# Performance work log

Measured on AMD Instinct MI355X. Metric: run time of the kernel, lower is better.

The kernel has to match this reference:

```python
import jax, jax.numpy as jnp
import numpy as np

N_ROI = 1024
N_CLASS = 21      # num_classes + 1
APP_DIM = 1024
D_F = 128
N_REL = 16
DIM_K = 64
DIM_G = 64


def loc2bbox(src, loc):
    # src, loc: [M,4] with (y0,x0,y1,x1) / (dy,dx,dh,dw)
    h = src[:, 2] - src[:, 0]
    w = src[:, 3] - src[:, 1]
    cy = src[:, 0] + 0.5 * h
    cx = src[:, 1] + 0.5 * w
    ncy = loc[:, 0] * h + cy
    ncx = loc[:, 1] * w + cx
    nh = jnp.exp(loc[:, 2]) * h
    nw = jnp.exp(loc[:, 3]) * w
    return jnp.stack([ncy - 0.5 * nh, ncx - 0.5 * nw,
                      ncy + 0.5 * nh, ncx + 0.5 * nw], axis=1)


def rank_embedding(n, feat_dim, wave_len=1000.0):
    rank = jnp.arange(n, dtype=jnp.float32)[:, None]
    fr = jnp.arange(feat_dim // 2, dtype=jnp.float32)
    dim_mat = 1.0 / (wave_len ** (fr / (feat_dim / 2.0)))
    mul = rank * dim_mat[None, :]
    return jnp.concatenate([jnp.sin(mul), jnp.cos(mul)], axis=-1)  # [n, feat_dim]


def positional_embedding(f_g, dim_g, wave_len=1000.0):
    # f_g: [N,4]; replicates the repo's PositionalEmbedding exactly
    x_min, y_min, x_max, y_max = jnp.split(f_g, 4, axis=1)  # [N,1] each
    cx = (x_min + x_max) * 0.5
    cy = (y_min + y_max) * 0.5
    w = (x_max - x_min) + 1.0
    h = (y_max - y_min) + 1.0
    dx = jnp.log(jnp.maximum(jnp.abs((cx - cx.T) / w), 1e-3))
    dy = jnp.log(jnp.maximum(jnp.abs((cy - cy.T) / h), 1e-3))
    dw = jnp.log(w / w.T)
    dh = jnp.log(h / h.T)
    pos = jnp.stack([dx, dy, dw, dh], axis=-1)               # [N,N,4]
    fr = jnp.arange(dim_g // 8, dtype=jnp.float32)
    dim_mat = 1.0 / (wave_len ** (fr / (dim_g / 8.0)))       # [dim_g/8]
    mul = (100.0 * pos)[..., None] * dim_mat                 # [N,N,4,dim_g/8]
    mul = mul.reshape(pos.shape[0], pos.shape[1], -1)
    return jnp.concatenate([jnp.sin(mul), jnp.cos(mul)], axis=-1)  # [N,N,dim_g]


def setup_inputs():
    key = jax.random.key(0)
    ks = jax.random.split(key, 16)
    yx = jax.random.uniform(ks[0], (N_ROI, 2), minval=0.0, maxval=500.0)
    hw = jax.random.uniform(ks[1], (N_ROI, 2), minval=16.0, maxval=128.0)
    sample_roi = jnp.concatenate([yx, yx + hw], axis=1)      # valid (y0,x0,y1,x1)
    roi_cls_loc = jax.random.normal(ks[2], (N_ROI, N_CLASS * 4)) * 0.5
    roi_score = jax.random.normal(ks[3], (N_ROI, N_CLASS))
    # force no background argmax -> nonzero() filter keeps all N (static shapes)
    roi_score = roi_score.at[:, 0].add(-10.0)
    appearance_features = jax.random.normal(ks[4], (N_ROI, APP_DIM))
    size = jnp.array([600, 800], dtype=jnp.int32)
    s = 0.02
    rank_w = jax.random.normal(ks[5], (APP_DIM, D_F)) * s
    rank_b = jnp.zeros((D_F,), jnp.float32)
    feat_w = jax.random.normal(ks[6], (APP_DIM, D_F)) * s
    feat_b = jnp.zeros((D_F,), jnp.float32)
    logit_w = jax.random.normal(ks[7], (APP_DIM, 1)) * s
    logit_b = jnp.zeros((1,), jnp.float32)
    wg_w = jax.random.normal(ks[8], (N_REL, DIM_G)) * s
    wg_b = jnp.full((N_REL,), 0.1, jnp.float32)  # keep some geo weights > 0
    wk_w = jax.random.normal(ks[9], (N_REL, D_F, DIM_K)) * s
    wk_b = jnp.zeros((N_REL, DIM_K), jnp.float32)
    wq_w = jax.random.normal(ks[10], (N_REL, D_F, DIM_K)) * s
    wq_b = jnp.zeros((N_REL, DIM_K), jnp.float32)
    wv_w = jax.random.normal(ks[11], (N_REL, D_F, DIM_K)) * s
    wv_b = jnp.zeros((N_REL, DIM_K), jnp.float32)
    return {"sample_roi": sample_roi, "roi_cls_loc": roi_cls_loc,
            "roi_score": roi_score, "appearance_features": appearance_features,
            "size": size,
            "rank_w": rank_w, "rank_b": rank_b, "feat_w": feat_w, "feat_b": feat_b,
            "logit_w": logit_w, "logit_b": logit_b,
            "wg_w": wg_w, "wg_b": wg_b, "wk_w": wk_w, "wk_b": wk_b,
            "wq_w": wq_w, "wq_b": wq_b, "wv_w": wv_w, "wv_b": wv_b}


def reference(sample_roi, roi_cls_loc, roi_score, appearance_features, size,
              rank_w, rank_b, feat_w, feat_b, logit_w, logit_b,
              wg_w, wg_b, wk_w, wk_b, wq_w, wq_b, wv_w, wv_b):
    n = sample_roi.shape[0]
    size_f = size.astype(jnp.float32)
    # loc denormalization (mean = 0)
    std = jnp.tile(jnp.array([0.1, 0.1, 0.2, 0.2], jnp.float32), N_CLASS)
    loc = (roi_cls_loc * std).reshape(-1, 4)                  # [N*21,4]
    roi_rep = jnp.broadcast_to(sample_roi[:, None, :], (n, N_CLASS, 4)).reshape(-1, 4)
    cls_bbox = loc2bbox(roi_rep, loc).reshape(n, N_CLASS, 4)
    # replicates original's clamp on class-strided slices of the [N,21,4] view
    cls_bbox = cls_bbox.at[:, 0::2].set(jnp.clip(cls_bbox[:, 0::2], 0.0, size_f[0]))
    cls_bbox = cls_bbox.at[:, 1::2].set(jnp.clip(cls_bbox[:, 1::2], 0.0, size_f[1]))
    prob_all = jax.nn.softmax(roi_score, axis=1)
    prob = jnp.max(prob_all, axis=-1)
    prob_argmax = jnp.argmax(prob_all, axis=-1)
    cls_bbox = cls_bbox[jnp.arange(n), prob_argmax]           # [N,4]
    # background filter; inputs guarantee all foreground -> static size n
    nz = jnp.nonzero(prob_argmax, size=n, fill_value=0)[0]
    prob_argmax = prob_argmax[nz]
    prob = prob[nz]
    cls_bbox = cls_bbox[nz]
    feats = appearance_features[nz]
    order = jnp.argsort(-prob)                                # descending
    sorted_prob = prob[order]
    sorted_cls_bboxes = cls_bbox[order]
    sorted_labels = prob_argmax[order]
    sorted_features = feats[order]
    nms_rank = rank_embedding(n, APP_DIM) @ rank_w + rank_b   # [N,D_F]
    emb_feat = sorted_features @ feat_w + feat_b + nms_rank   # [N,D_F]
    pos_emb = positional_embedding(sorted_cls_bboxes, DIM_G)  # [N,N,DIM_G]
    # 16 independent RelationUnits, batched as heads h
    w_g = jax.nn.relu(jnp.einsum('mng,hg->hmn', pos_emb, wg_w) + wg_b[:, None, None])
    k = jnp.einsum('nd,hdk->hnk', emb_feat, wk_w) + wk_b[:, None, :]
    q = jnp.einsum('nd,hdk->hnk', emb_feat, wq_w) + wq_b[:, None, :]
    v = jnp.einsum('nd,hdk->hnk', emb_feat, wv_w) + wv_b[:, None, :]
    # scaled_dot[m,n] = k_m . q_n (row m is 'key', softmax over n) per original
    scores = jnp.einsum('hmk,hnk->hmn', k, q) / np.sqrt(DIM_K).astype(np.float32)
    w_mn = jax.nn.softmax(jnp.log(jnp.maximum(w_g, 1e-6)) + scores, axis=-1)
    rel = jnp.einsum('hmn,hnk->hmk', w_mn, v)                 # [H,N,K]
    rel = rel.transpose(1, 0, 2).reshape(n, N_REL * DIM_K) + sorted_features
    s1 = jax.nn.sigmoid(rel @ logit_w + logit_b).reshape(-1)
    nms_scores = s1 * sorted_prob
    return nms_scores, sorted_labels - 1, sorted_cls_bboxes
```

## Files before the change

### kernel.cpp

```cpp
#include <hip/hip_runtime.h>
#include <hip/hip_bf16.h>
#include <math.h>

typedef unsigned long long u64;
typedef unsigned int u32;
typedef __hip_bfloat16 bf16;

#define N 1024
#define NCLS 21
#define APP 1024
#define DF 128
#define NH 16
#define DK 64
#define NS 2

typedef __attribute__((ext_vector_type(8))) short short8v;
typedef __attribute__((ext_vector_type(4))) float float4v;
union U4S8 { uint4 u; short8v s; };

__device__ __forceinline__ float b2f(bf16 x) { return __bfloat162float(x); }
__device__ __forceinline__ ushort f2bu(float x) { bf16 b = __float2bfloat16(x); return *(ushort*)&b; }
__device__ __forceinline__ float bu2f(ushort u) { return __uint_as_float(((uint)u) << 16); }

__global__ void k_prep(const float* __restrict__ roi, const float* __restrict__ cls_loc,
                       const float* __restrict__ score, const int* __restrict__ size,
                       float* __restrict__ prob, int* __restrict__ label,
                       float* __restrict__ bbox, u64* __restrict__ keys)
{
    int i = blockIdx.x * 256 + threadIdx.x;
    if (i >= N) return;
    float s[NCLS];
    float mx = -1e30f; int am = 0;
    for (int c = 0; c < NCLS; c++) {
        s[c] = score[i * NCLS + c];
        if (s[c] > mx) { mx = s[c]; am = c; }
    }
    float sum = 0.f;
    for (int c = 0; c < NCLS; c++) sum += expf(s[c] - mx);
    float p = 1.0f / sum;

    float y0 = roi[i*4+0], x0 = roi[i*4+1];
    float y1 = roi[i*4+2], x1 = roi[i*4+3];
    float hh = y1 - y0, ww = x1 - x0;
    float cy = y0 + 0.5f * hh, cx = x0 + 0.5f * ww;
    float l0 = cls_loc[i*84 + am*4 + 0] * 0.1f;
    float l1 = cls_loc[i*84 + am*4 + 1] * 0.1f;
    float l2 = cls_loc[i*84 + am*4 + 2] * 0.2f;
    float l3 = cls_loc[i*84 + am*4 + 3] * 0.2f;
    float ncy = l0 * hh + cy, ncx = l1 * ww + cx;
    float nh = expf(l2) * hh, nw = expf(l3) * ww;
    float b0 = ncy - 0.5f * nh, b1 = ncx - 0.5f * nw;
    float b2v = ncy + 0.5f * nh, b3 = ncx + 0.5f * nw;
    float lim = ((am & 1) == 0) ? (float)size[0] : (float)size[1];
    b0  = fminf(fmaxf(b0, 0.f), lim);
    b1  = fminf(fmaxf(b1, 0.f), lim);
    b2v = fminf(fmaxf(b2v, 0.f), lim);
    b3  = fminf(fmaxf(b3, 0.f), lim);
    prob[i] = p; label[i] = am;
    bbox[i*4+0] = b0; bbox[i*4+1] = b1; bbox[i*4+2] = b2v; bbox[i*4+3] = b3;
    keys[i] = ((u64)(0xFFFFFFFFu - __float_as_uint(p)) << 32) | (u32)i;
}

__global__ void __launch_bounds__(256) k_rank(
        const u64* __restrict__ keys, const float* __restrict__ prob,
        const int* __restrict__ label, const float* __restrict__ bbox,
        int* __restrict__ order, float* __restrict__ sprob,
        float* __restrict__ sbbox, float* __restrict__ out)
{
    __shared__ u64 sk[N];
    int t = threadIdx.x;
    int i = blockIdx.x * 256 + t;
    for (int j = t; j < N; j += 256) sk[j] = keys[j];
    __syncthreads();
    u64 my = sk[i];
    int r = 0;
    for (int j = 0; j < N; j++) r += (sk[j] < my) ? 1 : 0;
    order[r] = i;
    sprob[r] = prob[i];
    float b0 = bbox[i*4+0], b1 = bbox[i*4+1], b2 = bbox[i*4+2], b3 = bbox[i*4+3];
    sbbox[r*4+0] = b0; sbbox[r*4+1] = b1; sbbox[r*4+2] = b2; sbbox[r*4+3] = b3;
    out[N + r] = (float)(label[i] - 1);
    out[2*N + r*4 + 0] = b0;
    out[2*N + r*4 + 1] = b1;
    out[2*N + r*4 + 2] = b2;
    out[2*N + r*4 + 3] = b3;
}

__global__ void __launch_bounds__(256) k_geoemb(
        const int* __restrict__ order, const float* __restrict__ app,
        const float* __restrict__ feat_w, const float* __restrict__ rank_w,
        float* __restrict__ part,
        const float* __restrict__ sbbox, const float* __restrict__ wgw,
        const float* __restrict__ wgb, bf16* __restrict__ lw)
{
    __shared__ __align__(16) char smem[45328];
    int bx = blockIdx.x, t = threadIdx.x;
    int w = t >> 6, l = t & 63, l15 = l & 15, quad = l >> 4;

    if (bx < 4096) {
        ushort (*sE)[72]  = (ushort(*)[72])smem;
        uint   (*sOut)[132] = (uint(*)[132])(smem + 36864);
        float* mbb = (float*)(smem + 45312);
        int m = bx >> 2, nc = bx & 3;

        if (t == 0) {
            float b0 = sbbox[m*4+0], b1 = sbbox[m*4+1], b2 = sbbox[m*4+2], b3 = sbbox[m*4+3];
            mbb[0] = (b0 + b2) * 0.5f; mbb[1] = (b1 + b3) * 0.5f;
            mbb[2] = b2 - b0 + 1.0f;   mbb[3] = b3 - b1 + 1.0f;
        }
        U4S8 Bg0, Bg1;
        #pragma unroll
        for (int j = 0; j < 8; j++) {
            ((ushort*)&Bg0)[j] = f2bu(wgw[l15*64 + quad*8 + j]);
            ((ushort*)&Bg1)[j] = f2bu(wgw[l15*64 + 32 + quad*8 + j]);
        }
        float bias = wgb[l15];
        __syncthreads();

        int n = nc * 256 + t;
        float b0 = sbbox[n*4+0], b1 = sbbox[n*4+1], b2 = sbbox[n*4+2], b3 = sbbox[n*4+3];
        float cxn = (b0 + b2) * 0.5f, cyn = (b1 + b3) * 0.5f;
        float wn = b2 - b0 + 1.0f, hn = b3 - b1 + 1.0f;
        float dx = __logf(fmaxf(fabsf((mbb[0] - cxn) / mbb[2]), 1e-3f));
        float dy = __logf(fmaxf(fabsf((mbb[1] - cyn) / mbb[3]), 1e-3f));
        float dw = __logf(mbb[2] / wn);
        float dh = __logf(mbb[3] / hn);
        float pos[4] = { dx, dy, dw, dh };
        const float dmt[8] = { 1.0f, 0.42169650342f, 0.177827941f, 0.0749894209f,
                               0.0316227766f, 0.01333521432f, 0.00562341325f, 0.00237137371f };
        float args[32];
        #pragma unroll
        for (int c = 0; c < 4; c++)
            #pragma unroll
            for (int f = 0; f < 8; f++) args[c*8 + f] = 100.0f * pos[c] * dmt[f];
        uint* rowp = (uint*)&sE[t][0];
        #pragma unroll
        for (int jj = 0; jj < 16; jj++) {
            float s0 = __sinf(args[2*jj]), s1 = __sinf(args[2*jj+1]);
            rowp[jj] = (uint)f2bu(s0) | ((uint)f2bu(s1) << 16);
        }
        #pragma unroll
        for (int jj = 0; jj < 16; jj++) {
            float c0 = __cosf(args[2*jj]), c1 = __cosf(args[2*jj+1]);
            rowp[16 + jj] = (uint)f2bu(c0) | ((uint)f2bu(c1) << 16);
        }
        __syncthreads();

        #pragma unroll
        for (int mt2 = 0; mt2 < 4; mt2++) {
            int prow = w*64 + mt2*16 + l15;
            U4S8 Af0, Af1;
            Af0.u = *(uint4*)&sE[prow][quad*8];
            Af1.u = *(uint4*)&sE[prow][32 + quad*8];
            float4v c = (float4v){0.f, 0.f, 0.f, 0.f};
            c = __builtin_amdgcn_mfma_f32_16x16x32_bf16(Af0.s, Bg0.s, c, 0, 0, 0);
            c = __builtin_amdgcn_mfma_f32_16x16x32_bf16(Af1.s, Bg1.s, c, 0, 0, 0);
            float v0 = __logf(fmaxf(fmaxf(c[0] + bias, 0.f), 1e-6f));
            float v1 = __logf(fmaxf(fmaxf(c[1] + bias, 0.f), 1e-6f));
            float v2 = __logf(fmaxf(fmaxf(c[2] + bias, 0.f), 1e-6f));
            float v3 = __logf(fmaxf(fmaxf(c[3] + bias, 0.f), 1e-6f));
            int pb = (w*64 + mt2*16 + quad*4) >> 1;
            sOut[l15][pb]     = (uint)f2bu(v0) | ((uint)f2bu(v1) << 16);
            sOut[l15][pb + 1] = (uint)f2bu(v2) | ((uint)f2bu(v3) << 16);
        }
        __syncthreads();
        uint* lwu = (uint*)lw;
        #pragma unroll
        for (int it = 0; it < 8; it++) {
            int idx = t + it * 256;
            int hh = idx >> 7, col = idx & 127;
            lwu[((size_t)hh << 19) + ((size_t)m << 9) + nc*128 + col] = sOut[hh][col];
        }
    } else {
        ushort (*sA)[72] = (ushort(*)[72])smem;
        ushort (*sW)[72] = (ushort(*)[72])(smem + 9216);
        int* sOrd = (int*)(smem + 27648);
        int idx0 = bx - 4096;
        int rt = idx0 & 15, dg = (idx0 >> 4) & 3, ph = idx0 >> 6;
        int r0 = rt * 64;
        if (t < 64) sOrd[t] = order[r0 + t];
        __syncthreads();

        const float* Wsrc = ph ? rank_w : feat_w;
        float4v acc[8];
        #pragma unroll
        for (int nb = 0; nb < 8; nb++) acc[nb] = (float4v){0.f, 0.f, 0.f, 0.f};

        for (int dc = dg * 4; dc < dg * 4 + 4; dc++) {
            int d0 = dc * 64;
            #pragma unroll
            for (int it = 0; it < 32; it++) {
                int idx = t + it * 256;
                int d = idx >> 7, c = idx & 127;
                sW[c][d] = f2bu(Wsrc[(size_t)(d0 + d) * 128 + c]);
            }
            if (ph == 0) {
                #pragma unroll
                for (int it = 0; it < 16; it++) {
                    int idx = t + it * 256;
                    int r = idx >> 6, d = idx & 63;
                    sA[r][d] = f2bu(app[(size_t)sOrd[r] * 1024 + d0 + d]);
                }
            } else {
                #pragma unroll
                for (int it = 0; it < 16; it++) {
                    int idx = t + it * 256;
                    int r = idx >> 6, d = idx & 63;
                    int dgl = d0 + d;
                    float irow = (float)(r0 + r);
                    float val;
                    if (dgl < 512) val = __sinf(irow * exp2f(-(float)dgl * 0.019464422f));
                    else           val = __cosf(irow * exp2f(-(float)(dgl - 512) * 0.019464422f));
                    sA[r][d] = f2bu(val);
                }
            }
            __syncthreads();
            U4S8 Af0, Af1;
            Af0.u = *(uint4*)&sA[w*16 + l15][quad*8];
            Af1.u = *(uint4*)&sA[w*16 + l15][32 + quad*8];
            #pragma unroll
            for (int nb = 0; nb < 8; nb++) {
                U4S8 Bf0, Bf1;
                Bf0.u = *(uint4*)&sW[nb*16 + l15][quad*8];
                Bf1.u = *(uint4*)&sW[nb*16 + l15][32 + quad*8];
                acc[nb] = __builtin_amdgcn_mfma_f32_16x16x32_bf16(Af0.s, Bf0.s, acc[nb], 0, 0, 0);
                acc[nb] = __builtin_amdgcn_mfma_f32_16x16x32_bf16(Af1.s, Bf1.s, acc[nb], 0, 0, 0);
            }
            __syncthreads();
        }
        #pragma unroll
        for (int reg = 0; reg < 4; reg++) {
            int row = r0 + w*16 + quad*4 + reg;
            #pragma unroll
            for (int nb = 0; nb < 8; nb++)
                part[(((size_t)ph * 4 + dg) * 1024 + row) * 128 + nb*16 + l15] = acc[nb][reg];
        }
    }
}

__global__ void k_embsum(const float* __restrict__ part,
                         const float* __restrict__ feat_b, const float* __restrict__ rank_b,
                         bf16* __restrict__ embb)
{
    int gid = blockIdx.x * 256 + threadIdx.x;
    int c = gid & 127;
    float acc = feat_b[c] + rank_b[c];
    #pragma unroll
    for (int p8 = 0; p8 < 8; p8++) acc += part[(size_t)p8 * 131072 + gid];
    embb[gid] = __float2bfloat16(acc);
}

__global__ void __launch_bounds__(256) k_qkv2(
        const bf16* __restrict__ embb,
        const float* __restrict__ wq, const float* __restrict__ bq,
        const float* __restrict__ wk, const float* __restrict__ bk,
        const float* __restrict__ wv, const float* __restrict__ bv,
        bf16* __restrict__ q, bf16* __restrict__ k, bf16* __restrict__ v)
{
    __shared__ ushort sWt[64][136];
    int t = threadIdx.x;
    int rt = blockIdx.x, h = blockIdx.y, mat = blockIdx.z;
    const float* W  = (mat == 0) ? wq : (mat == 1) ? wk : wv;
    const float* Bb = (mat == 0) ? bq : (mat == 1) ? bk : bv;
    bf16* Out       = (mat == 0) ? q  : (mat == 1) ? k  : v;

    #pragma unroll
    for (int i = 0; i < 32; i++) {
        int idx = t + i * 256;
        int d = idx >> 6, kk = idx & 63;
        sWt[kk][d] = f2bu(W[((size_t)h * 128 + d) * 64 + kk]);
    }
    int w = t >> 6, l = t & 63, l15 = l & 15, quad = l >> 4;
    float biasv[4];
    #pragma unroll
    for (int nb = 0; nb < 4; nb++) biasv[nb] = Bb[h * 64 + nb*16 + l15];
    __syncthreads();

    U4S8 Bf[4][4];
    #pragma unroll
    for (int nb = 0; nb < 4; nb++)
        #pragma unroll
        for (int kc = 0; kc < 4; kc++)
            Bf[nb][kc].u = *(uint4*)&sWt[nb*16 + l15][kc*32 + quad*8];

    const uint4* A4 = (const uint4*)embb;
    int r0 = rt * 128 + w * 32;
    ushort* outu = (ushort*)Out;
    for (int mb = 0; mb < 2; mb++) {
        int arow = r0 + mb*16 + l15;
        U4S8 Af[4];
        #pragma unroll
        for (int kc = 0; kc < 4; kc++) Af[kc].u = A4[(size_t)arow * 16 + kc*4 + quad];
        float4v acc[4];
        #pragma unroll
        for (int nb = 0; nb < 4; nb++) acc[nb] = (float4v){0.f, 0.f, 0.f, 0.f};
        #pragma unroll
        for (int kc = 0; kc < 4; kc++)
            #pragma unroll
            for (int nb = 0; nb < 4; nb++)
                acc[nb] = __builtin_amdgcn_mfma_f32_16x16x32_bf16(Af[kc].s, Bf[nb][kc].s, acc[nb], 0, 0, 0);
        #pragma unroll
        for (int reg = 0; reg < 4; reg++) {
            int orow = r0 + mb*16 + quad*4 + reg;
            #pragma unroll
            for (int nb = 0; nb < 4; nb++)
                outu[((size_t)h * N + orow) * 64 + nb*16 + l15] = f2bu(acc[nb][reg] + biasv[nb]);
        }
    }
}

__global__ void __launch_bounds__(256) k_attn4(
        const bf16* __restrict__ q, const bf16* __restrict__ kmat,
        const bf16* __restrict__ v, const bf16* __restrict__ lw,
        bf16* __restrict__ opartb, float* __restrict__ mpart, float* __restrict__ zpart)
{
    __shared__ uint sQu[64][36];
    __shared__ uint sVtu[64][36];
    __shared__ uint slwu[64][36];
    __shared__ uint sPu[4][16][36];

    int t = threadIdx.x;
    int mt = blockIdx.x, h = blockIdx.y, ns = blockIdx.z;
    int m0 = mt * 64;
    int w = t >> 6, l = t & 63, l15 = l & 15, quad = l >> 4;

    U4S8 kf0, kf1;
    {
        const uint4* k4 = (const uint4*)kmat;
        size_t krow = ((size_t)h * N + m0 + w*16 + l15) * 8;
        kf0.u = k4[krow + quad];
        kf1.u = k4[krow + 4 + quad];
    }

    float4v O[4];
    float M[4], Z[4];
    #pragma unroll
    for (int i = 0; i < 4; i++) {
        O[i] = (float4v){0.f, 0.f, 0.f, 0.f};
        M[i] = -1e30f; Z[i] = 0.f;
    }

    const uint* qsrc = (const uint*)q;
    const uint* vsrc = (const uint*)v;
    const uint* lwsrc = (const uint*)lw;

    for (int tile = ns * (16/NS); tile < (ns + 1) * (16/NS); tile++) {
        int n0 = tile * 64;
        #pragma unroll
        for (int i = 0; i < 8; i++) {
            int idx = t + i * 256;
            int nj = idx >> 5, kp = idx & 31;
            sQu[nj][kp] = qsrc[((size_t)h * N + n0 + nj) * 32 + kp];
        }
        #pragma unroll
        for (int i = 0; i < 4; i++) {
            int idx = t + i * 256;
            int a = idx & 31, nh2 = idx >> 5;
            uint g0 = vsrc[((size_t)h * N + n0 + 2*nh2) * 32 + a];
            uint g1 = vsrc[((size_t)h * N + n0 + 2*nh2 + 1) * 32 + a];
            sVtu[2*a][nh2]     = (g0 & 0xFFFFu) | (g1 << 16);
            sVtu[2*a + 1][nh2] = (g0 >> 16) | (g1 & 0xFFFF0000u);
        }
        #pragma unroll
        for (int i = 0; i < 8; i++) {
            int idx = t + i * 256;
            int mi = idx >> 5, np = idx & 31;
            slwu[mi][np] = lwsrc[((size_t)h << 19) + ((size_t)(m0 + mi) << 9) + (n0 >> 1) + np];
        }
        __syncthreads();

        float4v S[4];
        #pragma unroll
        for (int nb = 0; nb < 4; nb++) {
            U4S8 bq0, bq1;
            bq0.u = *(uint4*)&sQu[nb*16 + l15][quad*4];
            bq1.u = *(uint4*)&sQu[nb*16 + l15][16 + quad*4];
            float4v zz = (float4v){0.f, 0.f, 0.f, 0.f};
            float4v p0 = __builtin_amdgcn_mfma_f32_16x16x32_bf16(kf0.s, bq0.s, zz, 0, 0, 0);
            S[nb] = __builtin_amdgcn_mfma_f32_16x16x32_bf16(kf1.s, bq1.s, p0, 0, 0, 0);
        }
        ushort* pRow[4];
        #pragma unroll
        for (int r = 0; r < 4; r++) pRow[r] = (ushort*)&sPu[w][quad*4 + r][0];
        #pragma unroll
        for (int r = 0; r < 4; r++) {
            int mi = w*16 + quad*4 + r;
            float sv[4];
            #pragma unroll
            for (int nb = 0; nb < 4; nb++) {
                int col = nb*16 + l15;
                uint lu = slwu[mi][col >> 1];
                float lv = (col & 1) ? __uint_as_float(lu & 0xFFFF0000u)
                                     : __uint_as_float(lu << 16);
                sv[nb] = S[nb][r] * 0.125f + lv;
            }
            float rm = fmaxf(fmaxf(sv[0], sv[1]), fmaxf(sv[2], sv[3]));
            #pragma unroll
            for (int off = 1; off < 16; off <<= 1)
                rm = fmaxf(rm, __shfl_xor(rm, off, 64));
            float newM = fmaxf(M[r], rm);
            float pr[4], rs = 0.f;
            #pragma unroll
            for (int nb = 0; nb < 4; nb++) {
                pr[nb] = __expf(sv[nb] - newM);
                rs += pr[nb];
            }
            #pragma unroll
            for (int off = 1; off < 16; off <<= 1)
                rs += __shfl_xor(rs, off, 64);
            float sc = __expf(M[r] - newM);
            M[r] = newM;
            Z[r] = Z[r] * sc + rs;
            #pragma unroll
            for (int kvb = 0; kvb < 4; kvb++) O[kvb][r] *= sc;
            #pragma unroll
            for (int nb = 0; nb < 4; nb++)
                pRow[r][nb*16 + l15] = f2bu(pr[nb]);
        }
        {
            U4S8 ap0, ap1;
            ap0.u = *(uint4*)&sPu[w][l15][quad*4];
            ap1.u = *(uint4*)&sPu[w][l15][16 + quad*4];
            #pragma unroll
            for (int kvb = 0; kvb < 4; kvb++) {
                U4S8 bv0, bv1;
                bv0.u = *(uint4*)&sVtu[kvb*16 + l15][quad*4];
                bv1.u = *(uint4*)&sVtu[kvb*16 + l15][16 + quad*4];
                O[kvb] = __builtin_amdgcn_mfma_f32_16x16x32_bf16(ap0.s, bv0.s, O[kvb], 0, 0, 0);
                O[kvb] = __builtin_amdgcn_mfma_f32_16x16x32_bf16(ap1.s, bv1.s, O[kvb], 0, 0, 0);
            }
        }
        __syncthreads();
    }

    ushort* ob = (ushort*)opartb;
    #pragma unroll
    for (int r = 0; r < 4; r++) {
        int m = m0 + w*16 + quad*4 + r;
        size_t row = ((size_t)ns * NH + h) * N + m;
        #pragma unroll
        for (int kvb = 0; kvb < 4; kvb++)
            ob[row * 64 + kvb*16 + l15] = f2bu(O[kvb][r]);
        if (l15 == 0) { mpart[row] = M[r]; zpart[row] = Z[r]; }
    }
}

__global__ void __launch_bounds__(128) k_final2(
        const bf16* __restrict__ opartb, const float* __restrict__ mpart,
        const float* __restrict__ zpart, const int* __restrict__ order,
        const float* __restrict__ app, const float* __restrict__ lw,
        const float* __restrict__ lb, const float* __restrict__ sprob,
        float* __restrict__ out)
{
    __shared__ float sWgt[NH][NS];
    __shared__ float sInvZ[NH];
    __shared__ float red[2];
    int m = blockIdx.x, t = threadIdx.x;
    if (t < NH) {
        int h = t;
        float Ms[NS], Mg = -1e30f;
        #pragma unroll
        for (int ns = 0; ns < NS; ns++) {
            Ms[ns] = mpart[(size_t)ns * 16384 + h * 1024 + m];
            Mg = fmaxf(Mg, Ms[ns]);
        }
        float Zt = 0.f;
        #pragma unroll
        for (int ns = 0; ns < NS; ns++) {
            float wgt = __expf(Ms[ns] - Mg);
            sWgt[h][ns] = wgt;
            Zt += zpart[(size_t)ns * 16384 + h * 1024 + m] * wgt;
        }
        sInvZ[h] = 1.0f / Zt;
    }
    __syncthreads();
    int o = order[m];
    const ushort* ob = (const ushort*)opartb;
    float s = 0.f;
    for (int j = t; j < APP; j += 128) {
        int hh = j >> 6, kk = j & 63;
        size_t base = ((size_t)hh * 1024 + m) * 64 + kk;
        float val = 0.f;
        #pragma unroll
        for (int ns = 0; ns < NS; ns++)
            val += bu2f(ob[(size_t)ns * 1048576 + base]) * sWgt[hh][ns];
        float rv = val * sInvZ[hh] + app[o * APP + j];
        s += rv * lw[j];
    }
    #pragma unroll
    for (int off = 32; off > 0; off >>= 1) s += __shfl_down(s, off, 64);
    if ((t & 63) == 0) red[t >> 6] = s;
    __syncthreads();
    if (t == 0) {
        float tot = red[0] + red[1] + lb[0];
        float s1 = 1.0f / (1.0f + expf(-tot));
        out[m] = s1 * sprob[m];
    }
}

extern "C" void kernel_launch(void* const* d_in, const int* in_sizes, int n_in,
                              void* d_out, int out_size, void* d_ws, size_t ws_size,
                              hipStream_t stream)
{
    const float* roi      = (const float*)d_in[0];
    const float* cls_loc  = (const float*)d_in[1];
    const float* score    = (const float*)d_in[2];
    const float* app      = (const float*)d_in[3];
    const int*   size     = (const int*)d_in[4];
    const float* rank_w   = (const float*)d_in[5];
    const float* rank_b   = (const float*)d_in[6];
    const float* feat_w   = (const float*)d_in[7];
    const float* feat_b   = (const float*)d_in[8];
    const float* logit_w  = (const float*)d_in[9];
    const float* logit_b  = (const float*)d_in[10];
    const float* wg_w     = (const float*)d_in[11];
    const float* wg_b     = (const float*)d_in[12];
    const float* wk_w     = (const float*)d_in[13];
    const float* wk_b     = (const float*)d_in[14];
    const float* wq_w     = (const float*)d_in[15];
    const float* wq_b     = (const float*)d_in[16];
    const float* wv_w     = (const float*)d_in[17];
    const float* wv_b     = (const float*)d_in[18];
    float* out = (float*)d_out;

    char* ws = (char*)d_ws;
    float* prob  = (float*)(ws + 0);
    int*   label = (int*)  (ws + 4096);
    float* bbox  = (float*)(ws + 8192);
    u64*   keys  = (u64*)  (ws + 24576);
    int*   order = (int*)  (ws + 32768);
    float* sprob = (float*)(ws + 36864);
    float* sbbox = (float*)(ws + 40960);
    bf16*  embb  = (bf16*) (ws + 57344);
    bf16*  q     = (bf16*) (ws + 8970240);
    bf16*  k     = (bf16*) (ws + 11067392);
    bf16*  v     = (bf16*) (ws + 13164544);
    bf16*  lwbuf = (bf16*) (ws + 17358848);
    float* part  = (float*)(ws + 50913280);
    bf16*  opartb= (bf16*) (ws + 67690496);
    float* mpart = (float*)(ws + 84467712);
    float* zpart = (float*)(ws + 84729856);

    k_prep<<<4, 256, 0, stream>>>(roi, cls_loc, score, size, prob, label, bbox, keys);
    k_rank<<<4, 256, 0, stream>>>(keys, prob, label, bbox, order, sprob, sbbox, out);
    k_geoemb<<<4224, 256, 0, stream>>>(order, app, feat_w, rank_w, part,
                                       sbbox, wg_w, wg_b, lwbuf);
    k_embsum<<<512, 256, 0, stream>>>(part, feat_b, rank_b, embb);
    k_qkv2<<<dim3(8, 16, 3), 256, 0, stream>>>(embb, wq_w, wq_b, wk_w, wk_b, wv_w, wv_b, q, k, v);
    k_attn4<<<dim3(16, 16, NS), 256, 0, stream>>>(q, k, v, lwbuf, opartb, mpart, zpart);
    k_final2<<<1024, 128, 0, stream>>>(opartb, mpart, zpart, order, app, logit_w, logit_b, sprob, out);
}
```

Measured before the change: 184.2 us.

## Compute positional embedding directly in MFMA operand registers, skipping LDS staging

The geometric-embedding blocks now generate the sin/cos embedding fragments directly in the registers each lane feeds to the MFMA, instead of writing per-row embeddings to shared memory and reading them back. Each lane computes only the single log-ratio coordinate its quad needs, cutting redundant log and sin work, and the two barriers plus the shared mbb staging are removed. Shared memory shrinks, which may allow more blocks per CU, and the output store is widened to 64-bit. The cost is that the bbox for row n is loaded redundantly across quads, and the sOut row padding changed from 132 to 133, which may misalign the paired uint2 reads.

```diff
diff --git a/kernel.cpp b/kernel.cpp
--- a/kernel.cpp
+++ b/kernel.cpp
@@ -93,21 +93,19 @@
         const float* __restrict__ sbbox, const float* __restrict__ wgw,
         const float* __restrict__ wgb, bf16* __restrict__ lw)
 {
-    __shared__ __align__(16) char smem[45328];
+    __shared__ __align__(16) char smem[27904];
     int bx = blockIdx.x, t = threadIdx.x;
     int w = t >> 6, l = t & 63, l15 = l & 15, quad = l >> 4;
 
     if (bx < 4096) {
-        ushort (*sE)[72]  = (ushort(*)[72])smem;
-        uint   (*sOut)[132] = (uint(*)[132])(smem + 36864);
-        float* mbb = (float*)(smem + 45312);
+        uint (*sOut)[133] = (uint(*)[133])smem;
         int m = bx >> 2, nc = bx & 3;
 
-        if (t == 0) {
-            float b0 = sbbox[m*4+0], b1 = sbbox[m*4+1], b2 = sbbox[m*4+2], b3 = sbbox[m*4+3];
-            mbb[0] = (b0 + b2) * 0.5f; mbb[1] = (b1 + b3) * 0.5f;
-            mbb[2] = b2 - b0 + 1.0f;   mbb[3] = b3 - b1 + 1.0f;
-        }
+        float mb0 = sbbox[m*4+0], mb1 = sbbox[m*4+1];
+        float mb2 = sbbox[m*4+2], mb3 = sbbox[m*4+3];
+        float cxm = (mb0 + mb2) * 0.5f, cym = (mb1 + mb3) * 0.5f;
+        float wm = mb2 - mb0 + 1.0f,   hm = mb3 - mb1 + 1.0f;
+
         U4S8 Bg0, Bg1;
         #pragma unroll
         for (int j = 0; j < 8; j++) {
@@ -115,43 +113,32 @@
             ((ushort*)&Bg1)[j] = f2bu(wgw[l15*64 + 32 + quad*8 + j]);
         }
         float bias = wgb[l15];
-        __syncthreads();
-
-        int n = nc * 256 + t;
-        float b0 = sbbox[n*4+0], b1 = sbbox[n*4+1], b2 = sbbox[n*4+2], b3 = sbbox[n*4+3];
-        float cxn = (b0 + b2) * 0.5f, cyn = (b1 + b3) * 0.5f;
-        float wn = b2 - b0 + 1.0f, hn = b3 - b1 + 1.0f;
-        float dx = __logf(fmaxf(fabsf((mbb[0] - cxn) / mbb[2]), 1e-3f));
-        float dy = __logf(fmaxf(fabsf((mbb[1] - cyn) / mbb[3]), 1e-3f));
-        float dw = __logf(mbb[2] / wn);
-        float dh = __logf(mbb[3] / hn);
-        float pos[4] = { dx, dy, dw, dh };
+
         const float dmt[8] = { 1.0f, 0.42169650342f, 0.177827941f, 0.0749894209f,
                                0.0316227766f, 0.01333521432f, 0.00562341325f, 0.00237137371f };
-        float args[32];
-        #pragma unroll
-        for (int c = 0; c < 4; c++)
-            #pragma unroll
-            for (int f = 0; f < 8; f++) args[c*8 + f] = 100.0f * pos[c] * dmt[f];
-        uint* rowp = (uint*)&sE[t][0];
-        #pragma unroll
-        for (int jj = 0; jj < 16; jj++) {
-            float s0 = __sinf(args[2*jj]), s1 = __sinf(args[2*jj+1]);
-            rowp[jj] = (uint)f2bu(s0) | ((uint)f2bu(s1) << 16);
-        }
-        #pragma unroll
-        for (int jj = 0; jj < 16; jj++) {
-            float c0 = __cosf(args[2*jj]), c1 = __cosf(args[2*jj+1]);
-            rowp[16 + jj] = (uint)f2bu(c0) | ((uint)f2bu(c1) << 16);
-        }
-        __syncthreads();
 
         #pragma unroll
         for (int mt2 = 0; mt2 < 4; mt2++) {
-            int prow = w*64 + mt2*16 + l15;
+            int n = nc*256 + w*64 + mt2*16 + l15;
+            float4 bb = *(const float4*)&sbbox[n*4];
+            float cxn = (bb.x + bb.z) * 0.5f, cyn = (bb.y + bb.w) * 0.5f;
+            float wn = bb.z - bb.x + 1.0f,    hn = bb.w - bb.y + 1.0f;
+            float num = (quad == 0) ? (cxm - cxn) : (quad == 1) ? (cym - cyn)
+                      : (quad == 2) ? wm : hm;
+            float den = (quad == 0) ? wm : (quad == 1) ? hm
+                      : (quad == 2) ? wn : hn;
+            float val = num / den;
+            val = (quad < 2) ? fmaxf(fabsf(val), 1e-3f) : val;
+            float p100 = 100.0f * __logf(val);
+
             U4S8 Af0, Af1;
-            Af0.u = *(uint4*)&sE[prow][quad*8];
-            Af1.u = *(uint4*)&sE[prow][32 + quad*8];
+            #pragma unroll
+            for (int j = 0; j < 8; j++) {
+                float a = p100 * dmt[j];
+                ((ushort*)&Af0)[j] = f2bu(__sinf(a));
+                ((ushort*)&Af1)[j] = f2bu(__cosf(a));
+            }
+
             float4v c = (float4v){0.f, 0.f, 0.f, 0.f};
             c = __builtin_amdgcn_mfma_f32_16x16x32_bf16(Af0.s, Bg0.s, c, 0, 0, 0);
             c = __builtin_amdgcn_mfma_f32_16x16x32_bf16(Af1.s, Bg1.s, c, 0, 0, 0);
@@ -166,10 +153,13 @@
         __syncthreads();
         uint* lwu = (uint*)lw;
         #pragma unroll
-        for (int it = 0; it < 8; it++) {
+        for (int it = 0; it < 4; it++) {
             int idx = t + it * 256;
-            int hh = idx >> 7, col = idx & 127;
-            lwu[((size_t)hh << 19) + ((size_t)m << 9) + nc*128 + col] = sOut[hh][col];
+            int hh = idx >> 6, col2 = idx & 63;
+            uint2 val;
+            val.x = sOut[hh][col2*2];
+            val.y = sOut[hh][col2*2 + 1];
+            *(uint2*)&lwu[((size_t)hh << 19) + ((size_t)m << 9) + nc*128 + col2*2] = val;
         }
     } else {
         ushort (*sA)[72] = (ushort(*)[72])smem;
```

Result: no change. 186.0 us (+1.0%).
